# Kernel tuning notes

Measured on AMD Instinct MI355X. Metric: run time of the kernel, lower is better.

## Reference

```python
import jax, jax.numpy as jnp
import numpy as np

BN_EPS = 1e-5


def spmm(rows, cols, vals, x):
    # Sparse [V,V] @ x for x: [B, V, F]. COO (rows, cols, vals) with E nnz.
    B, V, F = x.shape
    xt = jnp.transpose(x, (1, 0, 2)).reshape(V, B * F)      # [V, B*F]
    msg = xt[cols] * vals[:, None]                           # [E, B*F]
    y = jax.ops.segment_sum(msg, rows, num_segments=V)       # [V, B*F]
    return jnp.transpose(y.reshape(V, B, F), (1, 0, 2))      # [B, V, F]


def cheb_conv(rows, cols, vals, x, W, b):
    # Chebyshev graph conv: out = sum_k T_k(L) x @ W[k] + b ; W: [K, Fin, Fout]
    K = W.shape[0]
    x0 = x
    out = jnp.einsum('bvi,io->bvo', x0, W[0])
    if K > 1:
        x1 = spmm(rows, cols, vals, x0)
        out = out + jnp.einsum('bvi,io->bvo', x1, W[1])
        for k in range(2, K):
            x2 = 2.0 * spmm(rows, cols, vals, x1) - x0
            out = out + jnp.einsum('bvi,io->bvo', x2, W[k])
            x0, x1 = x1, x2
    return out + b


def bn_relu(x, gamma, beta):
    # BatchNorm1d (training stats) over (batch, nodes) per channel, then ReLU.
    m = jnp.mean(x, axis=(0, 1))
    v = jnp.var(x, axis=(0, 1))
    y = (x - m) * jax.lax.rsqrt(v + BN_EPS) * gamma + beta
    return jax.nn.relu(y)


def setup_inputs() -> dict:
    key = jax.random.key(0)
    ks = jax.random.split(key, 8)
    V, DEG, B, CIN, COUT = 49152, 20, 2, 128, 64
    x = jax.random.normal(ks[0], (B, V, CIN), dtype=jnp.float32)
    # HEALPix-like sparse Laplacian: diagonal + 20 random neighbors per node
    self_idx = jnp.arange(V, dtype=jnp.int32)
    nbr = jax.random.randint(ks[1], (V * DEG,), 0, V, dtype=jnp.int32)
    rows = jnp.concatenate([self_idx, jnp.repeat(self_idx, DEG)])
    cols = jnp.concatenate([self_idx, nbr])
    vals = jax.random.normal(ks[2], (V * (DEG + 1),), dtype=jnp.float32) * 0.1
    def w(k, shape):
        fan_in = shape[0] * shape[1]
        return jax.random.normal(k, shape, dtype=jnp.float32) * np.float32(np.sqrt(2.0 / fan_in))
    return {
        'x': x, 'rows': rows, 'cols': cols, 'vals': vals,
        'W1': w(ks[3], (1, CIN, COUT)), 'b1': jnp.zeros((COUT,), jnp.float32),
        'g1': jnp.ones((COUT,), jnp.float32), 'be1': jnp.zeros((COUT,), jnp.float32),
        'W2': w(ks[4], (3, COUT, COUT)), 'b2': jnp.zeros((COUT,), jnp.float32),
        'g2': jnp.ones((COUT,), jnp.float32), 'be2': jnp.zeros((COUT,), jnp.float32),
        'W3': w(ks[5], (1, COUT, CIN)), 'b3': jnp.zeros((CIN,), jnp.float32),
        'g3': jnp.ones((CIN,), jnp.float32), 'be3': jnp.zeros((CIN,), jnp.float32),
    }


def reference(x, rows, cols, vals, W1, b1, g1, be1, W2, b2, g2, be2, W3, b3, g3, be3):
    h = bn_relu(cheb_conv(rows, cols, vals, x, W1, b1), g1, be1)   # [B,V,64]
    h = bn_relu(cheb_conv(rows, cols, vals, h, W2, b2), g2, be2)   # [B,V,64]
    h = bn_relu(cheb_conv(rows, cols, vals, h, W3, b3), g3, be3)   # [B,V,128]
    return h
```

## Files before the change

kernel.cpp:

```cpp
#include <hip/hip_runtime.h>

#define VN 49152
#define DEG 20
#define NB 2
#define MROWS (NB * VN)

static constexpr float BN_EPS = 1e-5f;

typedef short bf16x8 __attribute__((ext_vector_type(8)));
typedef float floatx4 __attribute__((ext_vector_type(4)));

__device__ __forceinline__ unsigned short f2bf(float f) {
  unsigned int u = __builtin_bit_cast(unsigned int, f);
  u += 0x7FFFu + ((u >> 16) & 1u);
  return (unsigned short)(u >> 16);
}
__device__ __forceinline__ float bf2f(unsigned short h) {
  unsigned int u = ((unsigned int)h) << 16;
  return __builtin_bit_cast(float, u);
}
__device__ __forceinline__ float bflo(unsigned int u) {
  return __builtin_bit_cast(float, u << 16);
}
__device__ __forceinline__ float bfhi(unsigned int u) {
  return __builtin_bit_cast(float, u & 0xFFFF0000u);
}
__device__ __forceinline__ unsigned int packbf(float a, float b) {
  return (unsigned int)f2bf(a) | ((unsigned int)f2bf(b) << 16);
}

__device__ __forceinline__ void scsh_from(const float* __restrict__ gsum,
    const float* __restrict__ gamma, const float* __restrict__ beta,
    int c, int S, float& sc, float& sh) {
  float mean = gsum[c] * (1.f / MROWS);
  float var  = gsum[S + c] * (1.f / MROWS) - mean * mean;
  sc = gamma[c] * rsqrtf(var + BN_EPS);
  sh = beta[c] - mean * sc;
}

#define TRS 72

#define LDA1 136
__global__ __launch_bounds__(256) void gemm1(const float* __restrict__ X,
    const float* __restrict__ W, const float* __restrict__ bias,
    unsigned short* __restrict__ Y, float* __restrict__ gsum) {
  __shared__ unsigned short As[128 * LDA1];
  __shared__ unsigned short Bs[64 * LDA1];
  __shared__ float sred[128];
  int t = threadIdx.x;
  int row0 = blockIdx.x * 128;
  if (t < 128) sred[t] = 0.f;
  const float* Xt = X + (size_t)row0 * 128;
  #pragma unroll
  for (int c = 0; c < 16; ++c) {
    int f4i = c * 256 + t;
    int row = f4i >> 5, k = (f4i & 31) * 4;
    float4 v = *(const float4*)(Xt + row * 128 + k);
    unsigned int p0 = packbf(v.x, v.y);
    unsigned int p1 = packbf(v.z, v.w);
    *(uint2*)(&As[row * LDA1 + k]) = make_uint2(p0, p1);
  }
  #pragma unroll
  for (int c = 0; c < 32; ++c) {
    int f = c * 256 + t;
    int k = f >> 6, n = f & 63;
    Bs[n * LDA1 + k] = f2bf(W[f]);
  }
  __syncthreads();
  int l = t & 63, wv = t >> 6;
  int lr = l & 15, q = l >> 4;
  int m0 = wv * 32;
  floatx4 acc[2][4];
  #pragma unroll
  for (int mi = 0; mi < 2; ++mi)
    #pragma unroll
    for (int ni = 0; ni < 4; ++ni) acc[mi][ni] = (floatx4)(0.f);
  #pragma unroll
  for (int ks = 0; ks < 128; ks += 32) {
    bf16x8 af[2], bfr[4];
    #pragma unroll
    for (int mi = 0; mi < 2; ++mi)
      af[mi] = *(const bf16x8*)(&As[(m0 + mi * 16 + lr) * LDA1 + ks + q * 8]);
    #pragma unroll
    for (int ni = 0; ni < 4; ++ni)
      bfr[ni] = *(const bf16x8*)(&Bs[(ni * 16 + lr) * LDA1 + ks + q * 8]);
    #pragma unroll
    for (int mi = 0; mi < 2; ++mi)
      #pragma unroll
      for (int ni = 0; ni < 4; ++ni)
        acc[mi][ni] = __builtin_amdgcn_mfma_f32_16x16x32_bf16(af[mi], bfr[ni], acc[mi][ni], 0, 0, 0);
  }
  __syncthreads();
  int b = (row0 >= VN) ? 1 : 0;
  int b2 = b * 2, vb0 = row0 - b * VN;
  #pragma unroll
  for (int ni = 0; ni < 4; ++ni) {
    int col = ni * 16 + lr;
    float bv = bias[col];
    float s = 0.f, s2 = 0.f;
    #pragma unroll
    for (int mi = 0; mi < 2; ++mi)
      #pragma unroll
      for (int r = 0; r < 4; ++r) {
        float y = acc[mi][ni][r] + bv;
        s += y; s2 += y * y;
        As[(m0 + mi * 16 + q * 4 + r) * TRS + col] = f2bf(y);
      }
    atomicAdd(&sred[col], s);
    atomicAdd(&sred[64 + col], s2);
  }
  __syncthreads();
  #pragma unroll
  for (int i = 0; i < 4; ++i) {
    int idx = i * 256 + t;
    int p = idx >> 9, rem = idx & 511;
    int rowIdx = rem >> 2, ch0 = (rem & 3) * 8;
    uint4 d = *(const uint4*)(&As[rowIdx * TRS + p * 32 + ch0]);
    *(uint4*)(Y + ((size_t)(b2 + p) * VN + vb0 + rowIdx) * 32 + ch0) = d;
  }
  if (t < 128) atomicAdd(&gsum[t], sred[t]);
}

__global__ __launch_bounds__(256) void spmm1(const unsigned short* __restrict__ T1,
    const int* __restrict__ cols, const float* __restrict__ vals,
    const float* __restrict__ gsum, const float* __restrict__ gamma,
    const float* __restrict__ beta, unsigned short* __restrict__ X1out) {
  int g = blockIdx.x;
  int combo = (g & 7) >> 1;
  int rg = ((g >> 3) << 1) | (g & 1);
  int t = threadIdx.x;
  int wv = t >> 6, lane = t & 63;
  int v = rg * 64 + wv * 16 + (lane >> 2);
  int ch0 = (lane & 3) * 8;
  int cb = (combo & 1) * 32 + ch0;
  float sc[8], sh[8];
  #pragma unroll
  for (int j = 0; j < 8; ++j) scsh_from(gsum, gamma, beta, cb + j, 64, sc[j], sh[j]);
  const unsigned short* __restrict__ plane = T1 + (size_t)combo * VN * 32;
  float a[8];
  {
    float w0 = vals[v];
    uint4 d = *(const uint4*)(plane + (size_t)v * 32 + ch0);
    float e[8] = {bflo(d.x), bfhi(d.x), bflo(d.y), bfhi(d.y),
                  bflo(d.z), bfhi(d.z), bflo(d.w), bfhi(d.w)};
    #pragma unroll
    for (int j = 0; j < 8; ++j) {
      float h = fmaf(e[j], sc[j], sh[j]);
      h = h > 0.f ? h : 0.f;
      a[j] = w0 * h;
    }
  }
  const int*   __restrict__ cp = cols + VN + v * DEG;
  const float* __restrict__ vp = vals + VN + v * DEG;
  #pragma unroll
  for (int j = 0; j < DEG; ++j) {
    int cj = cp[j];
    float wj = vp[j];
    uint4 d = *(const uint4*)(plane + (size_t)cj * 32 + ch0);
    float e[8] = {bflo(d.x), bfhi(d.x), bflo(d.y), bfhi(d.y),
                  bflo(d.z), bfhi(d.z), bflo(d.w), bfhi(d.w)};
    #pragma unroll
    for (int i = 0; i < 8; ++i) {
      float h = fmaf(e[i], sc[i], sh[i]);
      h = h > 0.f ? h : 0.f;
      a[i] = fmaf(h, wj, a[i]);
    }
  }
  uint4 o;
  o.x = packbf(a[0], a[1]); o.y = packbf(a[2], a[3]);
  o.z = packbf(a[4], a[5]); o.w = packbf(a[6], a[7]);
  *(uint4*)(X1out + (size_t)combo * VN * 32 + (size_t)v * 32 + ch0) = o;
}

__global__ __launch_bounds__(256) void spmm2(const unsigned short* __restrict__ X1,
    const unsigned short* __restrict__ T1, const int* __restrict__ cols,
    const float* __restrict__ vals, const float* __restrict__ gsum,
    const float* __restrict__ gamma, const float* __restrict__ beta,
    unsigned short* __restrict__ X2out) {
  int g = blockIdx.x;
  int combo = (g & 7) >> 1;
  int rg = ((g >> 3) << 1) | (g & 1);
  int t = threadIdx.x;
  int wv = t >> 6, lane = t & 63;
  int v = rg * 64 + wv * 16 + (lane >> 2);
  int ch0 = (lane & 3) * 8;
  const size_t pbase = (size_t)combo * VN * 32;
  const size_t myoff = pbase + (size_t)v * 32 + ch0;
  const unsigned short* __restrict__ plane = X1 + pbase;
  float a[8];
  {
    float w0 = vals[v];
    uint4 d = *(const uint4*)(X1 + myoff);
    a[0] = w0 * bflo(d.x); a[1] = w0 * bfhi(d.x);
    a[2] = w0 * bflo(d.y); a[3] = w0 * bfhi(d.y);
    a[4] = w0 * bflo(d.z); a[5] = w0 * bfhi(d.z);
    a[6] = w0 * bflo(d.w); a[7] = w0 * bfhi(d.w);
  }
  const int*   __restrict__ cp = cols + VN + v * DEG;
  const float* __restrict__ vp = vals + VN + v * DEG;
  #pragma unroll
  for (int j = 0; j < DEG; ++j) {
    int cj = cp[j];
    float wj = vp[j];
    uint4 d = *(const uint4*)(plane + (size_t)cj * 32 + ch0);
    a[0] = fmaf(bflo(d.x), wj, a[0]); a[1] = fmaf(bfhi(d.x), wj, a[1]);
    a[2] = fmaf(bflo(d.y), wj, a[2]); a[3] = fmaf(bfhi(d.y), wj, a[3]);
    a[4] = fmaf(bflo(d.z), wj, a[4]); a[5] = fmaf(bfhi(d.z), wj, a[5]);
    a[6] = fmaf(bflo(d.w), wj, a[6]); a[7] = fmaf(bfhi(d.w), wj, a[7]);
  }
  int cb = (combo & 1) * 32 + ch0;
  float sc[8], sh[8];
  #pragma unroll
  for (int j = 0; j < 8; ++j) scsh_from(gsum, gamma, beta, cb + j, 64, sc[j], sh[j]);
  uint4 hr = *(const uint4*)(T1 + myoff);
  float e[8] = {bflo(hr.x), bfhi(hr.x), bflo(hr.y), bfhi(hr.y),
                bflo(hr.z), bfhi(hr.z), bflo(hr.w), bfhi(hr.w)};
  float oo[8];
  #pragma unroll
  for (int j = 0; j < 8; ++j) {
    float h = fmaf(e[j], sc[j], sh[j]);
    h = h > 0.f ? h : 0.f;
    oo[j] = 2.f * a[j] - h;
  }
  uint4 o;
  o.x = packbf(oo[0], oo[1]); o.y = packbf(oo[2], oo[3]);
  o.z = packbf(oo[4], oo[5]); o.w = packbf(oo[6], oo[7]);
  *(uint4*)(X2out + myoff) = o;
}

#define LDA2 72
__global__ __launch_bounds__(256) void gemm2(const unsigned short* X0,
    const unsigned short* __restrict__ X1, const unsigned short* __restrict__ X2,
    const float* __restrict__ W, const float* __restrict__ bias,
    const float* __restrict__ gsumIn, const float* __restrict__ gamma,
    const float* __restrict__ beta, unsigned short* Y,
    float* __restrict__ gsumOut) {
  __shared__ unsigned short As[128 * LDA2];
  __shared__ unsigned short Bs[64 * LDA2];
  __shared__ float sred[128];
  int t = threadIdx.x;
  int row0 = blockIdx.x * 128;
  int b = (row0 >= VN) ? 1 : 0;
  int b2 = b * 2;
  int vb0 = row0 - b * VN;
  if (t < 128) sred[t] = 0.f;
  int kk = (t & 15) * 4;
  int r0 = t >> 4;
  float tsc[4], tsh[4];
  #pragma unroll
  for (int j = 0; j < 4; ++j) scsh_from(gsumIn, gamma, beta, kk + j, 64, tsc[j], tsh[j]);
  int l = t & 63, wv = t >> 6;
  int lr = l & 15, q = l >> 4;
  int m0 = wv * 32;
  floatx4 acc[2][4];
  #pragma unroll
  for (int mi = 0; mi < 2; ++mi)
    #pragma unroll
    for (int ni = 0; ni < 4; ++ni) acc[mi][ni] = (floatx4)(0.f);

  #pragma unroll
  for (int term = 0; term < 3; ++term) {
    const unsigned short* Xp = (term == 0) ? X0 : (term == 1) ? X1 : X2;
    const float* Wt = W + term * 64 * 64;
    const unsigned short* srcBase =
        Xp + ((size_t)(b2 + (kk >> 5)) * VN + vb0) * 32 + (kk & 31);
    #pragma unroll
    for (int c8 = 0; c8 < 8; ++c8) {
      int row = c8 * 16 + r0;
      uint2 rawv = *(const uint2*)(srcBase + (size_t)row * 32);
      if (term == 0) {
        float y0 = fmaf(bflo(rawv.x), tsc[0], tsh[0]);
        float y1 = fmaf(bfhi(rawv.x), tsc[1], tsh[1]);
        float y2 = fmaf(bflo(rawv.y), tsc[2], tsh[2]);
        float y3 = fmaf(bfhi(rawv.y), tsc[3], tsh[3]);
        y0 = y0 > 0.f ? y0 : 0.f; y1 = y1 > 0.f ? y1 : 0.f;
        y2 = y2 > 0.f ? y2 : 0.f; y3 = y3 > 0.f ? y3 : 0.f;
        *(uint2*)(&As[row * LDA2 + kk]) = make_uint2(packbf(y0, y1), packbf(y2, y3));
      } else {
        *(uint2*)(&As[row * LDA2 + kk]) = rawv;
      }
    }
    #pragma unroll
    for (int c = 0; c < 16; ++c) {
      int f = c * 256 + t;
      int k = f >> 6, n = f & 63;
      Bs[n * LDA2 + k] = f2bf(Wt[f]);
    }
    __syncthreads();
    #pragma unroll
    for (int ks = 0; ks < 64; ks += 32) {
      bf16x8 af[2], bfr[4];
      #pragma unroll
      for (int mi = 0; mi < 2; ++mi)
        af[mi] = *(const bf16x8*)(&As[(m0 + mi * 16 + lr) * LDA2 + ks + q * 8]);
      #pragma unroll
      for (int ni = 0; ni < 4; ++ni)
        bfr[ni] = *(const bf16x8*)(&Bs[(ni * 16 + lr) * LDA2 + ks + q * 8]);
      #pragma unroll
      for (int mi = 0; mi < 2; ++mi)
        #pragma unroll
        for (int ni = 0; ni < 4; ++ni)
          acc[mi][ni] = __builtin_amdgcn_mfma_f32_16x16x32_bf16(af[mi], bfr[ni], acc[mi][ni], 0, 0, 0);
    }
    __syncthreads();
  }
  #pragma unroll
  for (int ni = 0; ni < 4; ++ni) {
    int col = ni * 16 + lr;
    float bv = bias[col];
    float s = 0.f, s2 = 0.f;
    #pragma unroll
    for (int mi = 0; mi < 2; ++mi)
      #pragma unroll
      for (int r = 0; r < 4; ++r) {
        float y = acc[mi][ni][r] + bv;
        s += y; s2 += y * y;
        As[(m0 + mi * 16 + q * 4 + r) * TRS + col] = f2bf(y);
      }
    atomicAdd(&sred[col], s);
    atomicAdd(&sred[64 + col], s2);
  }
  __syncthreads();
  #pragma unroll
  for (int i = 0; i < 4; ++i) {
    int idx = i * 256 + t;
    int p = idx >> 9, rem = idx & 511;
    int rowIdx = rem >> 2, ch0 = (rem & 3) * 8;
    uint4 d = *(const uint4*)(&As[rowIdx * TRS + p * 32 + ch0]);
    *(uint4*)(Y + ((size_t)(b2 + p) * VN + vb0 + rowIdx) * 32 + ch0) = d;
  }
  if (t < 128) atomicAdd(&gsumOut[t], sred[t]);
}

__global__ __launch_bounds__(256) void gemm3(const unsigned short* __restrict__ X,
    const float* __restrict__ W, const float* __restrict__ bias,
    const float* __restrict__ gsumIn, const float* __restrict__ gamma,
    const float* __restrict__ beta, unsigned short* __restrict__ Y,
    float* __restrict__ gsumOut) {
  __shared__ unsigned short As[128 * LDA2];
  __shared__ unsigned short Bs[64 * LDA2];
  __shared__ float sred[128];
  int t = threadIdx.x;
  int row0 = blockIdx.x * 128;
  int n0 = blockIdx.y * 64;
  int b = (row0 >= VN) ? 1 : 0;
  int b2 = b * 2;
  int vb0 = row0 - b * VN;
  if (t < 128) sred[t] = 0.f;
  int kk = (t & 15) * 4;
  int r0 = t >> 4;
  float tsc[4], tsh[4];
  #pragma unroll
  for (int j = 0; j < 4; ++j) scsh_from(gsumIn, gamma, beta, kk + j, 64, tsc[j], tsh[j]);
  const unsigned short* srcBase =
      X + ((size_t)(b2 + (kk >> 5)) * VN + vb0) * 32 + (kk & 31);
  #pragma unroll
  for (int c8 = 0; c8 < 8; ++c8) {
    int row = c8 * 16 + r0;
    uint2 rawv = *(const uint2*)(srcBase + (size_t)row * 32);
    float y0 = fmaf(bflo(rawv.x), tsc[0], tsh[0]);
    float y1 = fmaf(bfhi(rawv.x), tsc[1], tsh[1]);
    float y2 = fmaf(bflo(rawv.y), tsc[2], tsh[2]);
    float y3 = fmaf(bfhi(rawv.y), tsc[3], tsh[3]);
    y0 = y0 > 0.f ? y0 : 0.f; y1 = y1 > 0.f ? y1 : 0.f;
    y2 = y2 > 0.f ? y2 : 0.f; y3 = y3 > 0.f ? y3 : 0.f;
    *(uint2*)(&As[row * LDA2 + kk]) = make_uint2(packbf(y0, y1), packbf(y2, y3));
  }
  #pragma unroll
  for (int c = 0; c < 16; ++c) {
    int f = c * 256 + t;
    int k = f >> 6, n = f & 63;
    Bs[n * LDA2 + k] = f2bf(W[k * 128 + n0 + n]);
  }
  __syncthreads();
  int l = t & 63, wv = t >> 6;
  int lr = l & 15, q = l >> 4;
  int m0 = wv * 32;
  floatx4 acc[2][4];
  #pragma unroll
  for (int mi = 0; mi < 2; ++mi)
    #pragma unroll
    for (int ni = 0; ni < 4; ++ni) acc[mi][ni] = (floatx4)(0.f);
  #pragma unroll
  for (int ks = 0; ks < 64; ks += 32) {
    bf16x8 af[2], bfr[4];
    #pragma unroll
    for (int mi = 0; mi < 2; ++mi)
      af[mi] = *(const bf16x8*)(&As[(m0 + mi * 16 + lr) * LDA2 + ks + q * 8]);
    #pragma unroll
    for (int ni = 0; ni < 4; ++ni)
      bfr[ni] = *(const bf16x8*)(&Bs[(ni * 16 + lr) * LDA2 + ks + q * 8]);
    #pragma unroll
    for (int mi = 0; mi < 2; ++mi)
      #pragma unroll
      for (int ni = 0; ni < 4; ++ni)
        acc[mi][ni] = __builtin_amdgcn_mfma_f32_16x16x32_bf16(af[mi], bfr[ni], acc[mi][ni], 0, 0, 0);
  }
  __syncthreads();
  #pragma unroll
  for (int ni = 0; ni < 4; ++ni) {
    int lc = ni * 16 + lr;
    int col = n0 + lc;
    float bv = bias[col];
    float s = 0.f, s2 = 0.f;
    #pragma unroll
    for (int mi = 0; mi < 2; ++mi)
      #pragma unroll
      for (int r = 0; r < 4; ++r) {
        float y = acc[mi][ni][r] + bv;
        s += y; s2 += y * y;
        As[(m0 + mi * 16 + q * 4 + r) * TRS + lc] = f2bf(y);
      }
    atomicAdd(&sred[lc], s);
    atomicAdd(&sred[64 + lc], s2);
  }
  __syncthreads();
  #pragma unroll
  for (int i = 0; i < 4; ++i) {
    int idx = i * 256 + t;
    int rowIdx = idx >> 3, c0 = (idx & 7) * 8;
    uint4 d = *(const uint4*)(&As[rowIdx * TRS + c0]);
    *(uint4*)(Y + (size_t)(row0 + rowIdx) * 128 + n0 + c0) = d;
  }
  if (t < 128) {
    int lc = t & 63, p = t >> 6;
    atomicAdd(&gsumOut[p * 128 + n0 + lc], sred[t]);
  }
}

__global__ __launch_bounds__(256) void bn_apply_final(const unsigned short* __restrict__ T,
    float* __restrict__ Y, const float* __restrict__ gsum,
    const float* __restrict__ gamma, const float* __restrict__ beta) {
  size_t i4 = ((size_t)blockIdx.x * 256 + threadIdx.x) * 4;
  int c0 = (int)(i4 & 127);
  ushort4 tv = *(const ushort4*)(T + i4);
  unsigned short sv[4] = {tv.x, tv.y, tv.z, tv.w};
  float ov[4];
  #pragma unroll
  for (int j = 0; j < 4; ++j) {
    int c = c0 + j;
    float sc, sh;
    scsh_from(gsum, gamma, beta, c, 128, sc, sh);
    float y = fmaf(bf2f(sv[j]), sc, sh);
    ov[j] = y > 0.f ? y : 0.f;
  }
  *(float4*)(Y + i4) = make_float4(ov[0], ov[1], ov[2], ov[3]);
}

extern "C" void kernel_launch(void* const* d_in, const int* in_sizes, int n_in,
                              void* d_out, int out_size, void* d_ws, size_t ws_size,
                              hipStream_t stream) {
  const float* x    = (const float*)d_in[0];
  const int*   cols = (const int*)  d_in[2];
  const float* vals = (const float*)d_in[3];
  const float* W1   = (const float*)d_in[4];
  const float* b1   = (const float*)d_in[5];
  const float* g1   = (const float*)d_in[6];
  const float* be1  = (const float*)d_in[7];
  const float* W2   = (const float*)d_in[8];
  const float* b2   = (const float*)d_in[9];
  const float* g2   = (const float*)d_in[10];
  const float* be2  = (const float*)d_in[11];
  const float* W3   = (const float*)d_in[12];
  const float* b3   = (const float*)d_in[13];
  const float* g3   = (const float*)d_in[14];
  const float* be3  = (const float*)d_in[15];
  float* out = (float*)d_out;

  const size_t PL = (size_t)MROWS * 64;
  unsigned short* P0 = (unsigned short*)d_ws;
  unsigned short* P1 = P0 + PL;
  unsigned short* P2 = P1 + PL;
  float* ctrl  = (float*)(P2 + 2 * PL);
  float* gsum1 = ctrl;
  float* gsum2 = ctrl + 128;
  float* gsum3 = ctrl + 256;

  hipMemsetAsync(ctrl, 0, 512 * sizeof(float), stream);

  dim3 blk(256);
  int rowb = MROWS / 128;
  int spmm_blocks = 3072;
  int ap128_blocks = (int)(PL * 2 / 4 / 256);

  gemm1<<<rowb, blk, 0, stream>>>(x, W1, b1, P0, gsum1);

  spmm1<<<spmm_blocks, blk, 0, stream>>>(P0, cols, vals, gsum1, g1, be1, P1);
  spmm2<<<spmm_blocks, blk, 0, stream>>>(P1, P0, cols, vals, gsum1, g1, be1, P2);
  gemm2<<<rowb, blk, 0, stream>>>(P0, P1, P2, W2, b2, gsum1, g1, be1, P0, gsum2);

  dim3 g3grid(rowb, 2);
  gemm3<<<g3grid, blk, 0, stream>>>(P0, W3, b3, gsum2, g2, be2, P2, gsum3);
  bn_apply_final<<<ap128_blocks, blk, 0, stream>>>(P2, out, gsum3, g3, be3);
}
```

Measured before the change: 291.4 us.

## Fuse second Chebyshev SpMM into gemm2 and build the X2 tile in LDS

The standalone spmm2 kernel is removed. gemm2 now gathers neighbour rows of X1 itself, forms 2·L·X1 − relu(bn(X0)) for its 128-row tile and writes that tile straight into shared memory before the third MFMA pass. The BN scale/shift values are computed once per block into shared memory and reused. This avoids writing and re-reading the X2 intermediate in global memory and saves one kernel launch. In exchange the gather runs on far fewer threads (two per row instead of many small blocks), so there is less parallelism to hide gather latency, and register pressure and load imbalance inside gemm2 go up.

```diff
diff --git a/kernel.cpp b/kernel.cpp
--- a/kernel.cpp
+++ b/kernel.cpp
@@ -56,9 +56,7 @@
     int f4i = c * 256 + t;
     int row = f4i >> 5, k = (f4i & 31) * 4;
     float4 v = *(const float4*)(Xt + row * 128 + k);
-    unsigned int p0 = packbf(v.x, v.y);
-    unsigned int p1 = packbf(v.z, v.w);
-    *(uint2*)(&As[row * LDA1 + k]) = make_uint2(p0, p1);
+    *(uint2*)(&As[row * LDA1 + k]) = make_uint2(packbf(v.x, v.y), packbf(v.z, v.w));
   }
   #pragma unroll
   for (int c = 0; c < 32; ++c) {
@@ -172,65 +170,10 @@
   *(uint4*)(X1out + (size_t)combo * VN * 32 + (size_t)v * 32 + ch0) = o;
 }
 
-__global__ __launch_bounds__(256) void spmm2(const unsigned short* __restrict__ X1,
-    const unsigned short* __restrict__ T1, const int* __restrict__ cols,
-    const float* __restrict__ vals, const float* __restrict__ gsum,
-    const float* __restrict__ gamma, const float* __restrict__ beta,
-    unsigned short* __restrict__ X2out) {
-  int g = blockIdx.x;
-  int combo = (g & 7) >> 1;
-  int rg = ((g >> 3) << 1) | (g & 1);
-  int t = threadIdx.x;
-  int wv = t >> 6, lane = t & 63;
-  int v = rg * 64 + wv * 16 + (lane >> 2);
-  int ch0 = (lane & 3) * 8;
-  const size_t pbase = (size_t)combo * VN * 32;
-  const size_t myoff = pbase + (size_t)v * 32 + ch0;
-  const unsigned short* __restrict__ plane = X1 + pbase;
-  float a[8];
-  {
-    float w0 = vals[v];
-    uint4 d = *(const uint4*)(X1 + myoff);
-    a[0] = w0 * bflo(d.x); a[1] = w0 * bfhi(d.x);
-    a[2] = w0 * bflo(d.y); a[3] = w0 * bfhi(d.y);
-    a[4] = w0 * bflo(d.z); a[5] = w0 * bfhi(d.z);
-    a[6] = w0 * bflo(d.w); a[7] = w0 * bfhi(d.w);
-  }
-  const int*   __restrict__ cp = cols + VN + v * DEG;
-  const float* __restrict__ vp = vals + VN + v * DEG;
-  #pragma unroll
-  for (int j = 0; j < DEG; ++j) {
-    int cj = cp[j];
-    float wj = vp[j];
-    uint4 d = *(const uint4*)(plane + (size_t)cj * 32 + ch0);
-    a[0] = fmaf(bflo(d.x), wj, a[0]); a[1] = fmaf(bfhi(d.x), wj, a[1]);
-    a[2] = fmaf(bflo(d.y), wj, a[2]); a[3] = fmaf(bfhi(d.y), wj, a[3]);
-    a[4] = fmaf(bflo(d.z), wj, a[4]); a[5] = fmaf(bfhi(d.z), wj, a[5]);
-    a[6] = fmaf(bflo(d.w), wj, a[6]); a[7] = fmaf(bfhi(d.w), wj, a[7]);
-  }
-  int cb = (combo & 1) * 32 + ch0;
-  float sc[8], sh[8];
-  #pragma unroll
-  for (int j = 0; j < 8; ++j) scsh_from(gsum, gamma, beta, cb + j, 64, sc[j], sh[j]);
-  uint4 hr = *(const uint4*)(T1 + myoff);
-  float e[8] = {bflo(hr.x), bfhi(hr.x), bflo(hr.y), bfhi(hr.y),
-                bflo(hr.z), bfhi(hr.z), bflo(hr.w), bfhi(hr.w)};
-  float oo[8];
-  #pragma unroll
-  for (int j = 0; j < 8; ++j) {
-    float h = fmaf(e[j], sc[j], sh[j]);
-    h = h > 0.f ? h : 0.f;
-    oo[j] = 2.f * a[j] - h;
-  }
-  uint4 o;
-  o.x = packbf(oo[0], oo[1]); o.y = packbf(oo[2], oo[3]);
-  o.z = packbf(oo[4], oo[5]); o.w = packbf(oo[6], oo[7]);
-  *(uint4*)(X2out + myoff) = o;
-}
-
 #define LDA2 72
 __global__ __launch_bounds__(256) void gemm2(const unsigned short* X0,
-    const unsigned short* __restrict__ X1, const unsigned short* __restrict__ X2,
+    const unsigned short* __restrict__ X1,
+    const int* __restrict__ colsG, const float* __restrict__ valsG,
     const float* __restrict__ W, const float* __restrict__ bias,
     const float* __restrict__ gsumIn, const float* __restrict__ gamma,
     const float* __restrict__ beta, unsigned short* Y,
@@ -238,17 +181,23 @@
   __shared__ unsigned short As[128 * LDA2];
   __shared__ unsigned short Bs[64 * LDA2];
   __shared__ float sred[128];
+  __shared__ float scsh_s[128];
   int t = threadIdx.x;
   int row0 = blockIdx.x * 128;
   int b = (row0 >= VN) ? 1 : 0;
   int b2 = b * 2;
   int vb0 = row0 - b * VN;
   if (t < 128) sred[t] = 0.f;
+  if (t >= 128 && t < 192) {
+    int c = t - 128;
+    float sc, sh;
+    scsh_from(gsumIn, gamma, beta, c, 64, sc, sh);
+    scsh_s[c] = sc; scsh_s[64 + c] = sh;
+  }
+  __syncthreads();
+
   int kk = (t & 15) * 4;
   int r0 = t >> 4;
-  float tsc[4], tsh[4];
-  #pragma unroll
-  for (int j = 0; j < 4; ++j) scsh_from(gsumIn, gamma, beta, kk + j, 64, tsc[j], tsh[j]);
   int l = t & 63, wv = t >> 6;
   int lr = l & 15, q = l >> 4;
   int m0 = wv * 32;
@@ -258,33 +207,29 @@
     #pragma unroll
     for (int ni = 0; ni < 4; ++ni) acc[mi][ni] = (floatx4)(0.f);
 
-  #pragma unroll
-  for (int term = 0; term < 3; ++term) {
-    const unsigned short* Xp = (term == 0) ? X0 : (term == 1) ? X1 : X2;
-    const float* Wt = W + term * 64 * 64;
+  {
+    float tsc[4], tsh[4];
+    #pragma unroll
+    for (int j = 0; j < 4; ++j) { tsc[j] = scsh_s[kk + j]; tsh[j] = scsh_s[64 + kk + j]; }
     const unsigned short* srcBase =
-        Xp + ((size_t)(b2 + (kk >> 5)) * VN + vb0) * 32 + (kk & 31);
+        X0 + ((size_t)(b2 + (kk >> 5)) * VN + vb0) * 32 + (kk & 31);
     #pragma unroll
     for (int c8 = 0; c8 < 8; ++c8) {
       int row = c8 * 16 + r0;
       uint2 rawv = *(const uint2*)(srcBase + (size_t)row * 32);
-      if (term == 0) {
-        float y0 = fmaf(bflo(rawv.x), tsc[0], tsh[0]);
-        float y1 = fmaf(bfhi(rawv.x), tsc[1], tsh[1]);
-        float y2 = fmaf(bflo(rawv.y), tsc[2], tsh[2]);
-        float y3 = fmaf(bfhi(rawv.y), tsc[3], tsh[3]);
-        y0 = y0 > 0.f ? y0 : 0.f; y1 = y1 > 0.f ? y1 : 0.f;
-        y2 = y2 > 0.f ? y2 : 0.f; y3 = y3 > 0.f ? y3 : 0.f;
-        *(uint2*)(&As[row * LDA2 + kk]) = make_uint2(packbf(y0, y1), packbf(y2, y3));
-      } else {
-        *(uint2*)(&As[row * LDA2 + kk]) = rawv;
-      }
+      float y0 = fmaf(bflo(rawv.x), tsc[0], tsh[0]);
+      float y1 = fmaf(bfhi(rawv.x), tsc[1], tsh[1]);
+      float y2 = fmaf(bflo(rawv.y), tsc[2], tsh[2]);
+      float y3 = fmaf(bfhi(rawv.y), tsc[3], tsh[3]);
+      y0 = y0 > 0.f ? y0 : 0.f; y1 = y1 > 0.f ? y1 : 0.f;
+      y2 = y2 > 0.f ? y2 : 0.f; y3 = y3 > 0.f ? y3 : 0.f;
+      *(uint2*)(&As[row * LDA2 + kk]) = make_uint2(packbf(y0, y1), packbf(y2, y3));
     }
     #pragma unroll
     for (int c = 0; c < 16; ++c) {
       int f = c * 256 + t;
       int k = f >> 6, n = f & 63;
-      Bs[n * LDA2 + k] = f2bf(Wt[f]);
+      Bs[n * LDA2 + k] = f2bf(W[f]);
     }
     __syncthreads();
     #pragma unroll
@@ -304,6 +249,117 @@
     }
     __syncthreads();
   }
+
+  {
+    const unsigned short* srcBase =
+        X1 + ((size_t)(b2 + (kk >> 5)) * VN + vb0) * 32 + (kk & 31);
+    #pragma unroll
+    for (int c8 = 0; c8 < 8; ++c8) {
+      int row = c8 * 16 + r0;
+      *(uint2*)(&As[row * LDA2 + kk]) = *(const uint2*)(srcBase + (size_t)row * 32);
+    }
+    #pragma unroll
+    for (int c = 0; c < 16; ++c) {
+      int f = c * 256 + t;
+      int k = f >> 6, n = f & 63;
+      Bs[n * LDA2 + k] = f2bf(W[64 * 64 + f]);
+    }
+    __syncthreads();
+    #pragma unroll
+    for (int ks = 0; ks < 64; ks += 32) {
+      bf16x8 af[2], bfr[4];
+      #pragma unroll
+      for (int mi = 0; mi < 2; ++mi)
+        af[mi] = *(const bf16x8*)(&As[(m0 + mi * 16 + lr) * LDA2 + ks + q * 8]);
+      #pragma unroll
+      for (int ni = 0; ni < 4; ++ni)
+        bfr[ni] = *(const bf16x8*)(&Bs[(ni * 16 + lr) * LDA2 + ks + q * 8]);
+      #pragma unroll
+      for (int mi = 0; mi < 2; ++mi)
+        #pragma unroll
+        for (int ni = 0; ni < 4; ++ni)
+          acc[mi][ni] = __builtin_amdgcn_mfma_f32_16x16x32_bf16(af[mi], bfr[ni], acc[mi][ni], 0, 0, 0);
+    }
+    __syncthreads();
+  }
+
+  {
+    int row = t >> 1;
+    int half = t & 1;
+    int v = vb0 + row;
+    const unsigned short* plane = X1 + (size_t)(b2 + half) * VN * 32;
+    float a[4][8];
+    {
+      float w0 = valsG[v];
+      #pragma unroll
+      for (int g = 0; g < 4; ++g) {
+        uint4 d = *(const uint4*)(plane + (size_t)v * 32 + g * 8);
+        a[g][0] = w0 * bflo(d.x); a[g][1] = w0 * bfhi(d.x);
+        a[g][2] = w0 * bflo(d.y); a[g][3] = w0 * bfhi(d.y);
+        a[g][4] = w0 * bflo(d.z); a[g][5] = w0 * bfhi(d.z);
+        a[g][6] = w0 * bflo(d.w); a[g][7] = w0 * bfhi(d.w);
+      }
+    }
+    const int*   cp = colsG + VN + v * DEG;
+    const float* vp = valsG + VN + v * DEG;
+    #pragma unroll
+    for (int j = 0; j < DEG; ++j) {
+      int cj = cp[j];
+      float wj = vp[j];
+      const unsigned short* src = plane + (size_t)cj * 32;
+      #pragma unroll
+      for (int g = 0; g < 4; ++g) {
+        uint4 d = *(const uint4*)(src + g * 8);
+        a[g][0] = fmaf(bflo(d.x), wj, a[g][0]); a[g][1] = fmaf(bfhi(d.x), wj, a[g][1]);
+        a[g][2] = fmaf(bflo(d.y), wj, a[g][2]); a[g][3] = fmaf(bfhi(d.y), wj, a[g][3]);
+        a[g][4] = fmaf(bflo(d.z), wj, a[g][4]); a[g][5] = fmaf(bfhi(d.z), wj, a[g][5]);
+        a[g][6] = fmaf(bflo(d.w), wj, a[g][6]); a[g][7] = fmaf(bfhi(d.w), wj, a[g][7]);
+      }
+    }
+    const unsigned short* trow = X0 + ((size_t)(b2 + half) * VN + v) * 32;
+    #pragma unroll
+    for (int g = 0; g < 4; ++g) {
+      uint4 hr = *(const uint4*)(trow + g * 8);
+      int cb = half * 32 + g * 8;
+      float e[8] = {bflo(hr.x), bfhi(hr.x), bflo(hr.y), bfhi(hr.y),
+                    bflo(hr.z), bfhi(hr.z), bflo(hr.w), bfhi(hr.w)};
+      float oo[8];
+      #pragma unroll
+      for (int k = 0; k < 8; ++k) {
+        float h = fmaf(e[k], scsh_s[cb + k], scsh_s[64 + cb + k]);
+        h = h > 0.f ? h : 0.f;
+        oo[k] = 2.f * a[g][k] - h;
+      }
+      uint4 o;
+      o.x = packbf(oo[0], oo[1]); o.y = packbf(oo[2], oo[3]);
+      o.z = packbf(oo[4], oo[5]); o.w = packbf(oo[6], oo[7]);
+      *(uint4*)(&As[row * LDA2 + cb]) = o;
+    }
+    #pragma unroll
+    for (int c = 0; c < 16; ++c) {
+      int f = c * 256 + t;
+      int k = f >> 6, n = f & 63;
+      Bs[n * LDA2 + k] = f2bf(W[2 * 64 * 64 + f]);
+    }
+    __syncthreads();
+    #pragma unroll
+    for (int ks = 0; ks < 64; ks += 32) {
+      bf16x8 af[2], bfr[4];
+      #pragma unroll
+      for (int mi = 0; mi < 2; ++mi)
+        af[mi] = *(const bf16x8*)(&As[(m0 + mi * 16 + lr) * LDA2 + ks + q * 8]);
+      #pragma unroll
+      for (int ni = 0; ni < 4; ++ni)
+        bfr[ni] = *(const bf16x8*)(&Bs[(ni * 16 + lr) * LDA2 + ks + q * 8]);
+      #pragma unroll
+      for (int mi = 0; mi < 2; ++mi)
+        #pragma unroll
+        for (int ni = 0; ni < 4; ++ni)
+          acc[mi][ni] = __builtin_amdgcn_mfma_f32_16x16x32_bf16(af[mi], bfr[ni], acc[mi][ni], 0, 0, 0);
+    }
+    __syncthreads();
+  }
+
   #pragma unroll
   for (int ni = 0; ni < 4; ++ni) {
     int col = ni * 16 + lr;
@@ -486,8 +542,7 @@
   gemm1<<<rowb, blk, 0, stream>>>(x, W1, b1, P0, gsum1);
 
   spmm1<<<spmm_blocks, blk, 0, stream>>>(P0, cols, vals, gsum1, g1, be1, P1);
-  spmm2<<<spmm_blocks, blk, 0, stream>>>(P1, P0, cols, vals, gsum1, g1, be1, P2);
-  gemm2<<<rowb, blk, 0, stream>>>(P0, P1, P2, W2, b2, gsum1, g1, be1, P0, gsum2);
+  gemm2<<<rowb, blk, 0, stream>>>(P0, P1, cols, vals, W2, b2, gsum1, g1, be1, P0, gsum2);
 
   dim3 g3grid(rowb, 2);
   gemm3<<<g3grid, blk, 0, stream>>>(P0, W3, b3, gsum2, g2, be2, P2, gsum3);
```

After: 347.8 us. +19.4%, slower.
